# Performance work log

Measured on AMD Instinct MI355X. Metric: run time of the kernel, lower is better.

## Reference

```python
import jax, jax.numpy as jnp
import numpy as np

NUM_CLASSES = 2
THRESHOLD = 0.35
NEGPOS_RATIO = 3
VAR0, VAR1 = 0.1, 0.2
ALPHA = 1.0
B, P, G = 16, 131072, 64


def _iou(a, b):
    # a: [G,4] point-form gts, b: [P,4] point-form priors -> [G,P]
    tl = jnp.maximum(a[:, None, :2], b[None, :, :2])
    br = jnp.minimum(a[:, None, 2:], b[None, :, 2:])
    wh = jnp.clip(br - tl, 0.0)
    inter = wh[..., 0] * wh[..., 1]
    area_a = (a[:, 2] - a[:, 0]) * (a[:, 3] - a[:, 1])
    area_b = (b[:, 2] - b[:, 0]) * (b[:, 3] - b[:, 1])
    return inter / (area_a[:, None] + area_b[None, :] - inter)


def setup_inputs() -> dict:
    key = jax.random.key(0)
    k1, k2, k3, k4, k5, k6 = jax.random.split(key, 6)
    loc_preds = jax.random.normal(k1, (B, P, 4), jnp.float32)
    cls_preds = jax.random.normal(k2, (B, P, NUM_CLASSES), jnp.float32)
    # priors in center form [cx, cy, w, h]
    pcxy = jax.random.uniform(k3, (P, 2), jnp.float32)
    pwh = 0.02 + 0.15 * jax.random.uniform(k4, (P, 2), jnp.float32)
    priorbox = jnp.concatenate([pcxy, pwh], axis=1)
    # ground-truth boxes; stored as [y1,x1,y2,x2,label] so that the module's
    # column permutation [1,0,3,2] yields valid point-form [x1,y1,x2,y2]
    xy1 = 0.8 * jax.random.uniform(k5, (B, G, 2), jnp.float32)
    wh = 0.02 + 0.1 * jax.random.uniform(k6, (B, G, 2), jnp.float32)
    xy2 = xy1 + wh
    boxes_perm = jnp.stack([xy1[..., 1], xy1[..., 0], xy2[..., 1], xy2[..., 0]], axis=-1)
    labels = jnp.ones((B, G, 1), jnp.float32)  # single foreground class (face)
    targets = jnp.concatenate([boxes_perm, labels], axis=-1)
    return {"loc_preds": loc_preds, "cls_preds": cls_preds,
            "priorbox": priorbox, "targets": targets}


def _loss(loc_preds, cls_preds, priorbox, targets):
    priors_c = priorbox[: loc_preds.shape[1], :]
    priors_pt = jnp.concatenate(
        [priors_c[:, :2] - priors_c[:, 2:] / 2,
         priors_c[:, :2] + priors_c[:, 2:] / 2], axis=1)
    num_g = targets.shape[1]

    def match_one(t):
        gts = t[:, :4][:, jnp.array([1, 0, 3, 2])]  # -> point form [x1,y1,x2,y2]
        labels = t[:, 4]
        ov = _iou(gts, priors_pt)                    # [G,P]
        best_prior_idx = jnp.argmax(ov, axis=1)      # [G]
        bto = jnp.max(ov, axis=0)                    # [P] best gt overlap per prior
        bti = jnp.argmax(ov, axis=0)                 # [P]
        bto = bto.at[best_prior_idx].set(2.0)        # force best prior per gt
        bti = bti.at[best_prior_idx].set(jnp.arange(num_g))
        conf = jnp.where(bto < THRESHOLD, 0.0, labels[bti])
        m = gts[bti]                                 # [P,4] matched gt boxes
        g_cxcy = ((m[:, :2] + m[:, 2:]) / 2 - priors_c[:, :2]) / (VAR0 * priors_c[:, 2:])
        g_wh = jnp.log((m[:, 2:] - m[:, :2]) / priors_c[:, 2:]) / VAR1
        return conf, jnp.concatenate([g_cxcy, g_wh], axis=1)

    cls_batch, loc_batch = jax.vmap(match_one)(targets)
    cls_batch = jax.lax.stop_gradient(cls_batch)   # targets require no grad
    loc_batch = jax.lax.stop_gradient(loc_batch)

    pos = cls_batch > 0                              # [B,P]
    npos = jnp.sum(pos)

    # smooth-L1 over positive priors, mean over selected elements (size_average)
    d = loc_preds - loc_batch
    ad = jnp.abs(d)
    sl1 = jnp.where(ad < 1.0, 0.5 * d * d, ad - 0.5)
    loss_loc = jnp.sum(sl1 * pos[..., None]) / jnp.maximum(npos * 4, 1).astype(sl1.dtype)

    # per-prior CE loss for hard-negative mining
    ignore = cls_batch < 0
    lbl = jnp.where(ignore, 0.0, cls_batch).astype(jnp.int32)
    lse = jax.nn.logsumexp(cls_preds, axis=-1)       # [B,P]
    gathered = jnp.take_along_axis(cls_preds, lbl[..., None], axis=-1)[..., 0]
    loss_c = jnp.where(pos | ignore, 0.0, lse - gathered)
    # two-stage sort: rank of each prior by descending loss
    loss_idx = jnp.argsort(-loss_c, axis=1)
    idx_rank = jnp.argsort(loss_idx, axis=1)
    num_pos_img = jnp.sum(pos, axis=1, keepdims=True)
    num_neg = jnp.minimum(NEGPOS_RATIO * num_pos_img, pos.shape[1] - 1)
    neg = idx_rank < num_neg
    mask = pos | neg
    # cross-entropy over mined samples, mean over selected (size_average)
    loss_cls = jnp.sum((lse - gathered) * mask) / jnp.maximum(jnp.sum(mask), 1).astype(lse.dtype)

    loss = (loss_cls + ALPHA * loss_loc) / npos.astype(lse.dtype)
    return loss, loss_loc, loss_cls


def reference(loc_preds, cls_preds, priorbox, targets):
    return _loss(loc_preds, cls_preds, priorbox, targets)
```

## Files before the change

kernel.cpp:

```cpp
#include <hip/hip_runtime.h>

#define BB 16
#define PP 131072
#define GG 64
#define THRESH 0.35f
#define RMAX 0.086f
#define NCH 32
#define CPR 4096
#define NCT 16
#define CPT 8192

#define OFF_BESTP   0
#define OFF_H1TOT   262144
#define OFF_NPOSP   524288
#define OFF_PCP     526336
#define OFF_LOCP    528384
#define OFF_CIDX    530432
#define OFF_NEGS    530496
#define OFF_ARR     530560
#define OFF_DONE    530624
#define OFF_RESN    530688
#define OFF_RESK    530752
#define OFF_RESC    530816
#define OFF_RESL    530880
#define OFF_PU8     530944
#define OFF_KEYS    2628096
#define OFF_CAND    11016704

__global__ __launch_bounds__(1024, 8) void k_match(
    const float* __restrict__ priorbox, const float* __restrict__ targets,
    unsigned long long* __restrict__ bestp, unsigned char* __restrict__ pu8,
    unsigned* __restrict__ h1tot)
{
    __shared__ unsigned msk[8192];
    __shared__ float4 gxy[GG];
    __shared__ unsigned long long sbest[GG];
    const int b = blockIdx.y, chunk = blockIdx.x, tid = threadIdx.x;

    if (tid < 128) h1tot[b * 4096 + chunk * 128 + tid] = 0u;
    for (int i = tid; i < 8192; i += 1024) msk[i] = 0u;
    if (tid < GG) {
        const float* t = targets + (size_t)(b * GG + tid) * 5;
        gxy[tid] = make_float4(t[1], t[0], t[3], t[2]);
        sbest[tid] = 0ull;
    }
    __syncthreads();

    {
        const int g = tid & 63, strip = tid >> 6;
        float4 a = gxy[g];
        int cx0 = max(0, (int)((a.x - RMAX) * 64.f));
        int cx1 = min(63, (int)ceilf((a.z + RMAX) * 64.f) - 1);
        int cy0 = max(0, (int)((a.y - RMAX) * 64.f));
        int cy1 = min(63, (int)ceilf((a.w + RMAX) * 64.f) - 1);
        unsigned bit = 1u << (g & 31);
        const int word = (g >> 5);
        for (int cy = cy0 + strip; cy <= cy1; cy += 16)
            for (int cx = cx0; cx <= cx1; cx++)
                atomicOr(&msk[2 * (cy * 64 + cx) + word], bit);
    }
    __syncthreads();

#pragma unroll
    for (int j = 0; j < 4; j++) {
        const int p = chunk * CPR + j * 1024 + tid;
        float4 pr = *reinterpret_cast<const float4*>(priorbox + (size_t)p * 4);
        float hx = 0.5f * pr.z, hy = 0.5f * pr.w;
        float px1 = pr.x - hx, py1 = pr.y - hy;
        float px2 = pr.x + hx, py2 = pr.y + hy;
        float par = (px2 - px1) * (py2 - py1);
        int cx = min(63, max(0, (int)(pr.x * 64.f)));
        int cy = min(63, max(0, (int)(pr.y * 64.f)));
        uint2 mm = *reinterpret_cast<uint2*>(&msk[2 * (cy * 64 + cx)]);
        unsigned long long m = ((unsigned long long)mm.y << 32) | mm.x;
        const unsigned long long notp = (unsigned long long)(~(unsigned)p);
        float bv = -1.f; int bg = 0;
        while (m) {
            const int g0 = __ffsll(m) - 1; m &= m - 1;
            const bool has1 = (m != 0ull);
            const int g1 = has1 ? (__ffsll(m) - 1) : g0;
            if (has1) m &= m - 1;
            float4 a0 = gxy[g0];
            float4 a1 = gxy[g1];
            float w0 = fmaxf(fminf(a0.z, px2) - fmaxf(a0.x, px1), 0.f);
            float h0 = fmaxf(fminf(a0.w, py2) - fmaxf(a0.y, py1), 0.f);
            float w1 = fmaxf(fminf(a1.z, px2) - fmaxf(a1.x, px1), 0.f);
            float h1 = fmaxf(fminf(a1.w, py2) - fmaxf(a1.y, py1), 0.f);
            float ar0 = (a0.z - a0.x) * (a0.w - a0.y);
            float ar1 = (a1.z - a1.x) * (a1.w - a1.y);
            float i0 = w0 * h0, i1 = w1 * h1;
            float v0 = i0 * __builtin_amdgcn_rcpf(ar0 + par - i0);
            float v1 = i1 * __builtin_amdgcn_rcpf(ar1 + par - i1);
            if (v0 > bv) { bv = v0; bg = g0; }
            if (has1 && v1 > bv) { bv = v1; bg = g1; }
            if (v0 > 0.f)
                atomicMax(&sbest[g0],
                          (((unsigned long long)__float_as_uint(v0)) << 32) | notp);
            if (has1 && v1 > 0.f)
                atomicMax(&sbest[g1],
                          (((unsigned long long)__float_as_uint(v1)) << 32) | notp);
        }
        pu8[(size_t)b * PP + p] = (unsigned char)(bg | ((bv >= THRESH) ? 0x80 : 0));
    }

    __syncthreads();
    if (tid < GG) bestp[(b * NCH + chunk) * GG + tid] = sbest[tid];
}

__global__ __launch_bounds__(1024, 8) void k_loss(
    const float* __restrict__ loc_preds, const float* __restrict__ cls_preds,
    const float* __restrict__ priorbox, const float* __restrict__ targets,
    const unsigned long long* __restrict__ bestp, const unsigned char* __restrict__ pu8,
    unsigned* __restrict__ keys, unsigned* __restrict__ h1tot,
    int* __restrict__ nposp, float* __restrict__ pcp, float* __restrict__ locp,
    unsigned* __restrict__ cidx, float* __restrict__ negs,
    unsigned* __restrict__ arr, unsigned* __restrict__ done)
{
    __shared__ unsigned long long tmp64[2048];
    __shared__ unsigned hcnt[4096];
    __shared__ unsigned char ovr[CPR];
    __shared__ float4 gxy[GG];
    __shared__ float glab[GG];
    __shared__ float sred[32];
    __shared__ int sredi[16];
    const int b = blockIdx.y, chunk = blockIdx.x, tid = threadIdx.x;
    const int lane = tid & 63, wid = tid >> 6;

    if (tid == 0 && chunk == 0) {
        cidx[b] = 0u; negs[b] = 0.f; arr[b] = 0u;
        if (b == 0) *done = 0u;
    }

    tmp64[tid]        = bestp[(b * NCH + (tid >> 6)) * GG + (tid & 63)];
    tmp64[tid + 1024] = bestp[(b * NCH + 16 + (tid >> 6)) * GG + (tid & 63)];
    for (int i = tid; i < 4096; i += 1024) { hcnt[i] = 0u; ovr[i] = 0xFF; }
    if (tid < GG) {
        const float* t = targets + (size_t)(b * GG + tid) * 5;
        gxy[tid] = make_float4(t[1], t[0], t[3], t[2]);
        glab[tid] = t[4];
    }
    __syncthreads();
    for (int s = 16; s > 0; s >>= 1) {
        if (tid < s * 64) {
            const int c = tid >> 6, g = tid & 63;
            unsigned long long a = tmp64[c * 64 + g], d = tmp64[(c + s) * 64 + g];
            tmp64[c * 64 + g] = d > a ? d : a;
        }
        __syncthreads();
    }
    if (tid == 0) {
        for (int g = 0; g < GG; g++) {
            unsigned long long m = tmp64[g];
            if (m) {
                unsigned p = ~((unsigned)(m & 0xFFFFFFFFull));
                if ((int)(p >> 12) == chunk) ovr[p & (CPR - 1)] = (unsigned char)g;
            }
        }
    }
    __syncthreads();

    float locpart = 0.f, clspart = 0.f; int cnt = 0;
#pragma unroll
    for (int j = 0; j < 4; j++) {
        const int plocal = j * 1024 + tid;
        const size_t ip = (size_t)b * PP + chunk * CPR + plocal;
        const unsigned m8 = pu8[ip];
        int g = m8 & 63;
        bool pos = (m8 >> 7) != 0;
        const unsigned o = ovr[plocal];
        if (o != 0xFFu) { pos = true; g = (int)o; }
        const float2 cl = *reinterpret_cast<const float2*>(cls_preds + ip * 2);
        const float mx = fmaxf(cl.x, cl.y);
        const float lse = mx + log1pf(expf(fminf(cl.x, cl.y) - mx));
        unsigned key = 0u;
        if (pos && glab[g] > 0.f) {
            float gathered = (((int)glab[g]) == 0) ? cl.x : cl.y;
            clspart += lse - gathered;
            cnt++;
            const int p = chunk * CPR + plocal;
            float4 pr = *reinterpret_cast<const float4*>(priorbox + (size_t)p * 4);
            float4 gt = gxy[g];
            float gcx = ((gt.x + gt.z) * 0.5f - pr.x) / (0.1f * pr.z);
            float gcy = ((gt.y + gt.w) * 0.5f - pr.y) / (0.1f * pr.w);
            float gw = logf((gt.z - gt.x) / pr.z) / 0.2f;
            float gh = logf((gt.w - gt.y) / pr.w) / 0.2f;
            float4 lp = *reinterpret_cast<const float4*>(loc_preds + ip * 4);
            float d0 = lp.x - gcx, d1 = lp.y - gcy, d2 = lp.z - gw, d3 = lp.w - gh;
            float a0 = fabsf(d0), a1 = fabsf(d1), a2 = fabsf(d2), a3 = fabsf(d3);
            locpart += ((a0 < 1.f) ? 0.5f * d0 * d0 : a0 - 0.5f)
                     + ((a1 < 1.f) ? 0.5f * d1 * d1 : a1 - 0.5f)
                     + ((a2 < 1.f) ? 0.5f * d2 * d2 : a2 - 0.5f)
                     + ((a3 < 1.f) ? 0.5f * d3 * d3 : a3 - 0.5f);
        } else {
            float lc = lse - cl.x;
            key = __float_as_uint(lc);
            atomicAdd(&hcnt[key >> 20], 1u);
        }
        keys[ip] = key;
    }

    for (int o = 32; o; o >>= 1) {
        locpart += __shfl_xor(locpart, o);
        clspart += __shfl_xor(clspart, o);
        cnt     += __shfl_xor(cnt, o);
    }
    if (lane == 0) { sred[wid] = locpart; sred[16 + wid] = clspart; sredi[wid] = cnt; }
    __syncthreads();
    if (tid == 0) {
        float l = 0.f, c = 0.f; int n = 0;
        for (int i = 0; i < 16; i++) { l += sred[i]; c += sred[16 + i]; n += sredi[i]; }
        nposp[b * NCH + chunk] = n;
        pcp[b * NCH + chunk] = c;
        locp[b * NCH + chunk] = l;
    }
    __syncthreads();
    for (int i = tid; i < 4096; i += 1024) {
        unsigned cc = hcnt[i];
        if (cc) atomicAdd(&h1tot[b * 4096 + i], cc);
    }
}

template <int NBINS>
__device__ void find_kth_par(const unsigned* __restrict__ h, int k, int* sel, int* krem)
{
    constexpr int PER = NBINS / 1024;
    __shared__ unsigned wsum_[16];
    __shared__ int res_[2];
    const int tid = threadIdx.x, lane = tid & 63, wid = tid >> 6;
    __syncthreads();
    unsigned own[PER];
    unsigned s = 0;
#pragma unroll
    for (int i = 0; i < PER; i++) { own[i] = h[NBINS - 1 - (tid * PER + i)]; s += own[i]; }
    unsigned incl = s;
    for (int d = 1; d < 64; d <<= 1) {
        unsigned t = __shfl_up(incl, d);
        if (lane >= d) incl += t;
    }
    if (lane == 63) wsum_[wid] = incl;
    if (tid == 0) { res_[0] = -1; res_[1] = 0; }
    __syncthreads();
    unsigned woff = 0;
    for (int w = 0; w < 16; w++) woff += (w < wid) ? wsum_[w] : 0u;
    const unsigned texcl = woff + incl - s;
    if (k > 0 && texcl < (unsigned)k && texcl + s >= (unsigned)k) {
        unsigned run = texcl;
#pragma unroll
        for (int i = 0; i < PER; i++) {
            run += own[i];
            if (run >= (unsigned)k) {
                res_[0] = NBINS - 1 - (tid * PER + i);
                res_[1] = k - (int)(run - own[i]);
                break;
            }
        }
    }
    __syncthreads();
    *sel = res_[0]; *krem = res_[1];
}

__device__ float block_sum_f(float v)
{
    __shared__ float rs[16];
    const int tid = threadIdx.x;
    __syncthreads();
    for (int o = 32; o; o >>= 1) v += __shfl_xor(v, o);
    if ((tid & 63) == 0) rs[tid >> 6] = v;
    __syncthreads();
    float s = 0.f;
    for (int i = 0; i < 16; i++) s += rs[i];
    return s;
}

__global__ __launch_bounds__(1024) void k_tail(
    const unsigned* __restrict__ keys, const unsigned* __restrict__ h1tot,
    const int* __restrict__ nposp, const float* __restrict__ pcp,
    const float* __restrict__ locp, unsigned* __restrict__ cand,
    unsigned* __restrict__ cidx, float* __restrict__ negs,
    unsigned* __restrict__ arr, unsigned* __restrict__ done,
    int* __restrict__ resn, int* __restrict__ resk,
    float* __restrict__ resc, float* __restrict__ resl, float* __restrict__ out)
{
    __shared__ unsigned wcnt[16], wbase[16];
    __shared__ unsigned bbase;
    __shared__ int snp, lastflag;
    __shared__ unsigned ch[1024];
    __shared__ float cs[1024];
    const int b = blockIdx.y, chunk = blockIdx.x, tid = threadIdx.x;
    const int lane = tid & 63, wid = tid >> 6;

    if (tid == 0) {
        int np = 0;
        for (int c = 0; c < NCH; c++) np += nposp[b * NCH + c];
        snp = np;
    }
    unsigned kv[8];
#pragma unroll
    for (int j = 0; j < 8; j++)
        kv[j] = keys[(size_t)b * PP + chunk * CPT + j * 1024 + tid];
    __syncthreads();
    const int np = snp;
    const int k = min(3 * np, PP - 1);
    int sel1, kk1;
    find_kth_par<4096>(h1tot + b * 4096, k, &sel1, &kk1);
    const unsigned s1 = (unsigned)sel1;

    float nv = 0.f;
    if (sel1 >= 0) {
#pragma unroll
        for (int j = 0; j < 8; j++)
            if ((kv[j] >> 20) > s1) nv += __uint_as_float(kv[j]);
    }
    float nsum = block_sum_f(nv);
    if (tid == 0 && nsum != 0.f) atomicAdd(&negs[b], nsum);

    unsigned long long mv[8];
    unsigned wn = 0;
#pragma unroll
    for (int j = 0; j < 8; j++) {
        mv[j] = __ballot((kv[j] >> 20) == s1);
        wn += (unsigned)__popcll(mv[j]);
    }
    if (lane == 0) wcnt[wid] = wn;
    __syncthreads();
    if (tid == 0) {
        unsigned run = 0;
        for (int w = 0; w < 16; w++) { wbase[w] = run; run += wcnt[w]; }
        bbase = run ? atomicAdd(&cidx[b], run) : 0u;
    }
    __syncthreads();
    {
        unsigned run = bbase + wbase[wid];
        const unsigned long long lanemask = (1ull << lane) - 1ull;
#pragma unroll
        for (int j = 0; j < 8; j++) {
            if ((kv[j] >> 20) == s1)
                cand[(size_t)b * PP + run + (unsigned)__popcll(mv[j] & lanemask)] = kv[j];
            run += (unsigned)__popcll(mv[j]);
        }
    }

    __syncthreads();
    if (tid == 0) {
        __threadfence();
        unsigned old = atomicAdd(&arr[b], 1u);
        lastflag = (old == NCT - 1) ? 1 : 0;
    }
    __syncthreads();
    if (!lastflag) return;
    if (tid == 0) __threadfence();
    __syncthreads();

    const unsigned ncand = cidx[b];
    ch[tid] = 0u; cs[tid] = 0.f;
    __syncthreads();
    for (unsigned i = tid; i < ncand; i += 1024) {
        unsigned v = cand[(size_t)b * PP + i];
        unsigned bin = (v >> 10) & 1023u;
        atomicAdd(&ch[bin], 1u);
        atomicAdd(&cs[bin], __uint_as_float(v));
    }
    __syncthreads();
    int sel2, kk2;
    find_kth_par<1024>(ch, (sel1 < 0) ? 0 : kk1, &sel2, &kk2);
    float sumhi2 = block_sum_f((sel2 >= 0 && tid > sel2) ? cs[tid] : 0.f);

    __syncthreads();
    ch[tid] = 0u; cs[tid] = 0.f;
    __syncthreads();
    if (sel2 >= 0) {
        for (unsigned i = tid; i < ncand; i += 1024) {
            unsigned v = cand[(size_t)b * PP + i];
            if (((v >> 10) & 1023u) == (unsigned)sel2) {
                atomicAdd(&ch[v & 1023u], 1u);
                atomicAdd(&cs[v & 1023u], __uint_as_float(v));
            }
        }
    }
    __syncthreads();
    int sel3, needeq;
    find_kth_par<1024>(ch, (sel2 < 0) ? 0 : kk2, &sel3, &needeq);
    float sumhi3 = block_sum_f((sel3 >= 0 && tid > sel3) ? cs[tid] : 0.f);

    if (tid == 0) {
        float pcsum = 0.f, locsum = 0.f;
        for (int c = 0; c < NCH; c++) {
            pcsum += pcp[b * NCH + c];
            locsum += locp[b * NCH + c];
        }
        float add = 0.f;
        if (sel3 >= 0 && needeq > 0) {
            unsigned Kstar = ((unsigned)sel1 << 20) | ((unsigned)sel2 << 10) | (unsigned)sel3;
            add = needeq * __uint_as_float(Kstar);
        }
        resn[b] = np;
        resk[b] = k;
        resc[b] = pcsum + negs[b] + sumhi2 + sumhi3 + add;
        resl[b] = locsum;
        __threadfence();
        unsigned old = atomicAdd(done, 1u);
        lastflag = (old == BB - 1) ? 1 : 0;
    }
    __syncthreads();
    if (!lastflag || tid != 0) return;

    __threadfence();
    volatile int* vrn = (volatile int*)resn;
    volatile int* vrk = (volatile int*)resk;
    volatile float* vrc = (volatile float*)resc;
    volatile float* vrl = (volatile float*)resl;
    int npt = 0; long long maskc = 0; float clsnum = 0.f, locnum = 0.f;
    for (int b2 = 0; b2 < BB; b2++) {
        npt += vrn[b2];
        maskc += (long long)vrn[b2] + vrk[b2];
        clsnum += vrc[b2];
        locnum += vrl[b2];
    }
    float denom_loc = (float)((4 * npt > 1) ? 4 * npt : 1);
    float denom_cls = (float)((maskc > 1) ? maskc : 1);
    float loss_loc = locnum / denom_loc;
    float loss_cls = clsnum / denom_cls;
    out[0] = (loss_cls + loss_loc) / (float)npt;
    out[1] = loss_loc;
    out[2] = loss_cls;
}

extern "C" void kernel_launch(void* const* d_in, const int* in_sizes, int n_in,
                              void* d_out, int out_size, void* d_ws, size_t ws_size,
                              hipStream_t stream)
{
    const float* loc_preds = (const float*)d_in[0];
    const float* cls_preds = (const float*)d_in[1];
    const float* priorbox  = (const float*)d_in[2];
    const float* targets   = (const float*)d_in[3];
    float* out = (float*)d_out;

    char* ws = (char*)d_ws;
    unsigned long long* bestp = (unsigned long long*)(ws + OFF_BESTP);
    unsigned* h1tot = (unsigned*)(ws + OFF_H1TOT);
    int*      nposp = (int*)(ws + OFF_NPOSP);
    float*    pcp   = (float*)(ws + OFF_PCP);
    float*    locp  = (float*)(ws + OFF_LOCP);
    unsigned* cidx  = (unsigned*)(ws + OFF_CIDX);
    float*    negs  = (float*)(ws + OFF_NEGS);
    unsigned* arr   = (unsigned*)(ws + OFF_ARR);
    unsigned* done  = (unsigned*)(ws + OFF_DONE);
    int*      resn  = (int*)(ws + OFF_RESN);
    int*      resk  = (int*)(ws + OFF_RESK);
    float*    resc  = (float*)(ws + OFF_RESC);
    float*    resl  = (float*)(ws + OFF_RESL);
    unsigned char* pu8 = (unsigned char*)(ws + OFF_PU8);
    unsigned* keys  = (unsigned*)(ws + OFF_KEYS);
    unsigned* cand  = (unsigned*)(ws + OFF_CAND);

    k_match<<<dim3(NCH, BB), 1024, 0, stream>>>(priorbox, targets, bestp, pu8, h1tot);
    k_loss<<<dim3(NCH, BB), 1024, 0, stream>>>(loc_preds, cls_preds, priorbox, targets,
                                               bestp, pu8, keys, h1tot,
                                               nposp, pcp, locp, cidx, negs, arr, done);
    k_tail<<<dim3(NCT, BB), 1024, 0, stream>>>(keys, h1tot, nposp, pcp, locp, cand,
                                               cidx, negs, arr, done,
                                               resn, resk, resc, resl, out);
}
```

Measured before the change: 96.74 us.

## Split tail into separate kernels, shrink blocks to 256, coarsen match grid

Reworks the pipeline from three 1024-thread kernels into six smaller launches. k_match and k_loss move to 256-thread blocks over 64 chunks, and the match grid cell count drops from 64 to 32. The per-chunk best-prior reduction moves into a dedicated k_bred kernel. The last-block-done atomics in the tail are replaced by separate compact, select and final kernels. The aim is to improve occupancy and remove serial per-block reductions and atomic handshakes, at the cost of extra launch overhead and more IoU candidates per coarser grid cell.

```diff
diff --git a/kernel.cpp b/kernel.cpp
--- a/kernel.cpp
+++ b/kernel.cpp
@@ -5,40 +5,44 @@
 #define GG 64
 #define THRESH 0.35f
 #define RMAX 0.086f
-#define NCH 32
-#define CPR 4096
-#define NCT 16
-#define CPT 8192
+#define NCELL 32
+#define NCHM 64
+#define CPM 2048
+#define NCHL 64
+#define CPL 2048
+#define NCC 64
+#define CPC 2048
 
 #define OFF_BESTP   0
-#define OFF_H1TOT   262144
-#define OFF_NPOSP   524288
-#define OFF_PCP     526336
-#define OFF_LOCP    528384
-#define OFF_CIDX    530432
-#define OFF_NEGS    530496
-#define OFF_ARR     530560
-#define OFF_DONE    530624
-#define OFF_RESN    530688
-#define OFF_RESK    530752
-#define OFF_RESC    530816
-#define OFF_RESL    530880
-#define OFF_PU8     530944
-#define OFF_KEYS    2628096
-#define OFF_CAND    11016704
-
-__global__ __launch_bounds__(1024, 8) void k_match(
+#define OFF_BEST64  524288
+#define OFF_H1TOT   532480
+#define OFF_NPOSP   794624
+#define OFF_PCP     798720
+#define OFF_LOCP    802816
+#define OFF_CIDX    806912
+#define OFF_NEGS    806976
+#define OFF_RESN    807040
+#define OFF_RESK    807104
+#define OFF_RESC    807168
+#define OFF_RESL    807232
+#define OFF_PU8     807296
+#define OFF_KEYS    2904448
+#define OFF_CAND    11293056
+
+__global__ __launch_bounds__(256) void k_match(
     const float* __restrict__ priorbox, const float* __restrict__ targets,
     unsigned long long* __restrict__ bestp, unsigned char* __restrict__ pu8,
-    unsigned* __restrict__ h1tot)
-{
-    __shared__ unsigned msk[8192];
+    unsigned* __restrict__ h1tot, unsigned* __restrict__ cidx,
+    float* __restrict__ negs)
+{
+    __shared__ unsigned msk[2 * NCELL * NCELL];
     __shared__ float4 gxy[GG];
     __shared__ unsigned long long sbest[GG];
     const int b = blockIdx.y, chunk = blockIdx.x, tid = threadIdx.x;
 
-    if (tid < 128) h1tot[b * 4096 + chunk * 128 + tid] = 0u;
-    for (int i = tid; i < 8192; i += 1024) msk[i] = 0u;
+    if (tid < 64) h1tot[b * 4096 + chunk * 64 + tid] = 0u;
+    if (chunk == 0 && tid == 0) { cidx[b] = 0u; negs[b] = 0.f; }
+    for (int i = tid; i < 2 * NCELL * NCELL; i += 256) msk[i] = 0u;
     if (tid < GG) {
         const float* t = targets + (size_t)(b * GG + tid) * 5;
         gxy[tid] = make_float4(t[1], t[0], t[3], t[2]);
@@ -49,29 +53,29 @@
     {
         const int g = tid & 63, strip = tid >> 6;
         float4 a = gxy[g];
-        int cx0 = max(0, (int)((a.x - RMAX) * 64.f));
-        int cx1 = min(63, (int)ceilf((a.z + RMAX) * 64.f) - 1);
-        int cy0 = max(0, (int)((a.y - RMAX) * 64.f));
-        int cy1 = min(63, (int)ceilf((a.w + RMAX) * 64.f) - 1);
+        int cx0 = max(0, (int)((a.x - RMAX) * (float)NCELL));
+        int cx1 = min(NCELL - 1, (int)ceilf((a.z + RMAX) * (float)NCELL) - 1);
+        int cy0 = max(0, (int)((a.y - RMAX) * (float)NCELL));
+        int cy1 = min(NCELL - 1, (int)ceilf((a.w + RMAX) * (float)NCELL) - 1);
         unsigned bit = 1u << (g & 31);
         const int word = (g >> 5);
-        for (int cy = cy0 + strip; cy <= cy1; cy += 16)
+        for (int cy = cy0 + strip; cy <= cy1; cy += 4)
             for (int cx = cx0; cx <= cx1; cx++)
-                atomicOr(&msk[2 * (cy * 64 + cx) + word], bit);
-    }
-    __syncthreads();
-
-#pragma unroll
-    for (int j = 0; j < 4; j++) {
-        const int p = chunk * CPR + j * 1024 + tid;
+                atomicOr(&msk[2 * (cy * NCELL + cx) + word], bit);
+    }
+    __syncthreads();
+
+#pragma unroll
+    for (int j = 0; j < 8; j++) {
+        const int p = chunk * CPM + j * 256 + tid;
         float4 pr = *reinterpret_cast<const float4*>(priorbox + (size_t)p * 4);
         float hx = 0.5f * pr.z, hy = 0.5f * pr.w;
         float px1 = pr.x - hx, py1 = pr.y - hy;
         float px2 = pr.x + hx, py2 = pr.y + hy;
         float par = (px2 - px1) * (py2 - py1);
-        int cx = min(63, max(0, (int)(pr.x * 64.f)));
-        int cy = min(63, max(0, (int)(pr.y * 64.f)));
-        uint2 mm = *reinterpret_cast<uint2*>(&msk[2 * (cy * 64 + cx)]);
+        int cx = min(NCELL - 1, max(0, (int)(pr.x * (float)NCELL)));
+        int cy = min(NCELL - 1, max(0, (int)(pr.y * (float)NCELL)));
+        uint2 mm = *reinterpret_cast<uint2*>(&msk[2 * (cy * NCELL + cx)]);
         unsigned long long m = ((unsigned long long)mm.y << 32) | mm.x;
         const unsigned long long notp = (unsigned long long)(~(unsigned)p);
         float bv = -1.f; int bg = 0;
@@ -104,71 +108,66 @@
     }
 
     __syncthreads();
-    if (tid < GG) bestp[(b * NCH + chunk) * GG + tid] = sbest[tid];
-}
-
-__global__ __launch_bounds__(1024, 8) void k_loss(
+    if (tid < GG) bestp[(b * NCHM + chunk) * GG + tid] = sbest[tid];
+}
+
+__global__ void k_bred(const unsigned long long* __restrict__ bestp,
+                       unsigned long long* __restrict__ best64)
+{
+    const int b = blockIdx.x, g = threadIdx.x;
+    unsigned long long m = 0ull;
+#pragma unroll 8
+    for (int c = 0; c < NCHM; c++) {
+        unsigned long long v = bestp[(b * NCHM + c) * GG + g];
+        m = v > m ? v : m;
+    }
+    best64[b * GG + g] = m;
+}
+
+__global__ __launch_bounds__(256) void k_loss(
     const float* __restrict__ loc_preds, const float* __restrict__ cls_preds,
     const float* __restrict__ priorbox, const float* __restrict__ targets,
-    const unsigned long long* __restrict__ bestp, const unsigned char* __restrict__ pu8,
+    const unsigned long long* __restrict__ best64, const unsigned char* __restrict__ pu8,
     unsigned* __restrict__ keys, unsigned* __restrict__ h1tot,
-    int* __restrict__ nposp, float* __restrict__ pcp, float* __restrict__ locp,
-    unsigned* __restrict__ cidx, float* __restrict__ negs,
-    unsigned* __restrict__ arr, unsigned* __restrict__ done)
-{
-    __shared__ unsigned long long tmp64[2048];
+    int* __restrict__ nposp, float* __restrict__ pcp, float* __restrict__ locp)
+{
     __shared__ unsigned hcnt[4096];
-    __shared__ unsigned char ovr[CPR];
+    __shared__ unsigned ovr[CPL];
     __shared__ float4 gxy[GG];
     __shared__ float glab[GG];
-    __shared__ float sred[32];
-    __shared__ int sredi[16];
+    __shared__ float sred[8];
+    __shared__ int sredi[4];
     const int b = blockIdx.y, chunk = blockIdx.x, tid = threadIdx.x;
     const int lane = tid & 63, wid = tid >> 6;
 
-    if (tid == 0 && chunk == 0) {
-        cidx[b] = 0u; negs[b] = 0.f; arr[b] = 0u;
-        if (b == 0) *done = 0u;
-    }
-
-    tmp64[tid]        = bestp[(b * NCH + (tid >> 6)) * GG + (tid & 63)];
-    tmp64[tid + 1024] = bestp[(b * NCH + 16 + (tid >> 6)) * GG + (tid & 63)];
-    for (int i = tid; i < 4096; i += 1024) { hcnt[i] = 0u; ovr[i] = 0xFF; }
+    for (int i = tid; i < 4096; i += 256) hcnt[i] = 0u;
+    for (int i = tid; i < CPL; i += 256) ovr[i] = 0u;
     if (tid < GG) {
         const float* t = targets + (size_t)(b * GG + tid) * 5;
         gxy[tid] = make_float4(t[1], t[0], t[3], t[2]);
         glab[tid] = t[4];
     }
     __syncthreads();
-    for (int s = 16; s > 0; s >>= 1) {
-        if (tid < s * 64) {
-            const int c = tid >> 6, g = tid & 63;
-            unsigned long long a = tmp64[c * 64 + g], d = tmp64[(c + s) * 64 + g];
-            tmp64[c * 64 + g] = d > a ? d : a;
-        }
-        __syncthreads();
-    }
-    if (tid == 0) {
-        for (int g = 0; g < GG; g++) {
-            unsigned long long m = tmp64[g];
-            if (m) {
-                unsigned p = ~((unsigned)(m & 0xFFFFFFFFull));
-                if ((int)(p >> 12) == chunk) ovr[p & (CPR - 1)] = (unsigned char)g;
-            }
+    if (tid < GG) {
+        unsigned long long m = best64[b * GG + tid];
+        if (m) {
+            unsigned p = ~((unsigned)(m & 0xFFFFFFFFull));
+            if ((int)(p >> 11) == chunk)
+                atomicMax(&ovr[p & (CPL - 1)], (unsigned)tid + 1u);
         }
     }
     __syncthreads();
 
     float locpart = 0.f, clspart = 0.f; int cnt = 0;
 #pragma unroll
-    for (int j = 0; j < 4; j++) {
-        const int plocal = j * 1024 + tid;
-        const size_t ip = (size_t)b * PP + chunk * CPR + plocal;
+    for (int j = 0; j < 8; j++) {
+        const int plocal = j * 256 + tid;
+        const size_t ip = (size_t)b * PP + chunk * CPL + plocal;
         const unsigned m8 = pu8[ip];
         int g = m8 & 63;
         bool pos = (m8 >> 7) != 0;
         const unsigned o = ovr[plocal];
-        if (o != 0xFFu) { pos = true; g = (int)o; }
+        if (o) { pos = true; g = (int)o - 1; }
         const float2 cl = *reinterpret_cast<const float2*>(cls_preds + ip * 2);
         const float mx = fmaxf(cl.x, cl.y);
         const float lse = mx + log1pf(expf(fminf(cl.x, cl.y) - mx));
@@ -177,7 +176,7 @@
             float gathered = (((int)glab[g]) == 0) ? cl.x : cl.y;
             clspart += lse - gathered;
             cnt++;
-            const int p = chunk * CPR + plocal;
+            const int p = chunk * CPL + plocal;
             float4 pr = *reinterpret_cast<const float4*>(priorbox + (size_t)p * 4);
             float4 gt = gxy[g];
             float gcx = ((gt.x + gt.z) * 0.5f - pr.x) / (0.1f * pr.z);
@@ -204,17 +203,18 @@
         clspart += __shfl_xor(clspart, o);
         cnt     += __shfl_xor(cnt, o);
     }
-    if (lane == 0) { sred[wid] = locpart; sred[16 + wid] = clspart; sredi[wid] = cnt; }
+    if (lane == 0) { sred[wid] = locpart; sred[4 + wid] = clspart; sredi[wid] = cnt; }
     __syncthreads();
     if (tid == 0) {
-        float l = 0.f, c = 0.f; int n = 0;
-        for (int i = 0; i < 16; i++) { l += sred[i]; c += sred[16 + i]; n += sredi[i]; }
-        nposp[b * NCH + chunk] = n;
-        pcp[b * NCH + chunk] = c;
-        locp[b * NCH + chunk] = l;
-    }
-    __syncthreads();
-    for (int i = tid; i < 4096; i += 1024) {
+        float l = sred[0] + sred[1] + sred[2] + sred[3];
+        float c = sred[4] + sred[5] + sred[6] + sred[7];
+        int n = sredi[0] + sredi[1] + sredi[2] + sredi[3];
+        nposp[b * NCHL + chunk] = n;
+        pcp[b * NCHL + chunk] = c;
+        locp[b * NCHL + chunk] = l;
+    }
+    __syncthreads();
+    for (int i = tid; i < 4096; i += 256) {
         unsigned cc = hcnt[i];
         if (cc) atomicAdd(&h1tot[b * 4096 + i], cc);
     }
@@ -223,15 +223,14 @@
 template <int NBINS>
 __device__ void find_kth_par(const unsigned* __restrict__ h, int k, int* sel, int* krem)
 {
-    constexpr int PER = NBINS / 1024;
-    __shared__ unsigned wsum_[16];
+    constexpr int PER = NBINS / 256;
+    __shared__ unsigned wsum_[4];
     __shared__ int res_[2];
     const int tid = threadIdx.x, lane = tid & 63, wid = tid >> 6;
     __syncthreads();
-    unsigned own[PER];
     unsigned s = 0;
 #pragma unroll
-    for (int i = 0; i < PER; i++) { own[i] = h[NBINS - 1 - (tid * PER + i)]; s += own[i]; }
+    for (int i = 0; i < PER; i++) s += h[NBINS - 1 - (tid * PER + i)];
     unsigned incl = s;
     for (int d = 1; d < 64; d <<= 1) {
         unsigned t = __shfl_up(incl, d);
@@ -241,16 +240,16 @@
     if (tid == 0) { res_[0] = -1; res_[1] = 0; }
     __syncthreads();
     unsigned woff = 0;
-    for (int w = 0; w < 16; w++) woff += (w < wid) ? wsum_[w] : 0u;
+    for (int w = 0; w < 4; w++) woff += (w < wid) ? wsum_[w] : 0u;
     const unsigned texcl = woff + incl - s;
     if (k > 0 && texcl < (unsigned)k && texcl + s >= (unsigned)k) {
         unsigned run = texcl;
-#pragma unroll
         for (int i = 0; i < PER; i++) {
-            run += own[i];
+            unsigned hv = h[NBINS - 1 - (tid * PER + i)];
+            run += hv;
             if (run >= (unsigned)k) {
                 res_[0] = NBINS - 1 - (tid * PER + i);
-                res_[1] = k - (int)(run - own[i]);
+                res_[1] = k - (int)(run - hv);
                 break;
             }
         }
@@ -261,45 +260,44 @@
 
 __device__ float block_sum_f(float v)
 {
-    __shared__ float rs[16];
+    __shared__ float rs[4];
     const int tid = threadIdx.x;
     __syncthreads();
     for (int o = 32; o; o >>= 1) v += __shfl_xor(v, o);
     if ((tid & 63) == 0) rs[tid >> 6] = v;
     __syncthreads();
-    float s = 0.f;
-    for (int i = 0; i < 16; i++) s += rs[i];
-    return s;
-}
-
-__global__ __launch_bounds__(1024) void k_tail(
+    return rs[0] + rs[1] + rs[2] + rs[3];
+}
+
+__device__ int np_of_image(const int* __restrict__ nposp, int b)
+{
+    __shared__ int snp;
+    const int tid = threadIdx.x;
+    int v = (tid < 64) ? nposp[b * NCHL + tid] : 0;
+    if (tid < 64) {
+        for (int o = 32; o; o >>= 1) v += __shfl_xor(v, o);
+        if (tid == 0) snp = v;
+    }
+    __syncthreads();
+    return snp;
+}
+
+__global__ __launch_bounds__(256) void k_compact(
     const unsigned* __restrict__ keys, const unsigned* __restrict__ h1tot,
-    const int* __restrict__ nposp, const float* __restrict__ pcp,
-    const float* __restrict__ locp, unsigned* __restrict__ cand,
-    unsigned* __restrict__ cidx, float* __restrict__ negs,
-    unsigned* __restrict__ arr, unsigned* __restrict__ done,
-    int* __restrict__ resn, int* __restrict__ resk,
-    float* __restrict__ resc, float* __restrict__ resl, float* __restrict__ out)
-{
-    __shared__ unsigned wcnt[16], wbase[16];
+    const int* __restrict__ nposp, unsigned* __restrict__ cand,
+    unsigned* __restrict__ cidx, float* __restrict__ negs)
+{
+    __shared__ unsigned wcnt[4], wbase[4];
     __shared__ unsigned bbase;
-    __shared__ int snp, lastflag;
-    __shared__ unsigned ch[1024];
-    __shared__ float cs[1024];
     const int b = blockIdx.y, chunk = blockIdx.x, tid = threadIdx.x;
     const int lane = tid & 63, wid = tid >> 6;
 
-    if (tid == 0) {
-        int np = 0;
-        for (int c = 0; c < NCH; c++) np += nposp[b * NCH + c];
-        snp = np;
-    }
     unsigned kv[8];
 #pragma unroll
     for (int j = 0; j < 8; j++)
-        kv[j] = keys[(size_t)b * PP + chunk * CPT + j * 1024 + tid];
-    __syncthreads();
-    const int np = snp;
+        kv[j] = keys[(size_t)b * PP + chunk * CPC + j * 256 + tid];
+
+    const int np = np_of_image(nposp, b);
     const int k = min(3 * np, PP - 1);
     int sel1, kk1;
     find_kth_par<4096>(h1tot + b * 4096, k, &sel1, &kk1);
@@ -325,36 +323,46 @@
     __syncthreads();
     if (tid == 0) {
         unsigned run = 0;
-        for (int w = 0; w < 16; w++) { wbase[w] = run; run += wcnt[w]; }
+        for (int w = 0; w < 4; w++) { wbase[w] = run; run += wcnt[w]; }
         bbase = run ? atomicAdd(&cidx[b], run) : 0u;
     }
     __syncthreads();
-    {
-        unsigned run = bbase + wbase[wid];
-        const unsigned long long lanemask = (1ull << lane) - 1ull;
-#pragma unroll
-        for (int j = 0; j < 8; j++) {
-            if ((kv[j] >> 20) == s1)
-                cand[(size_t)b * PP + run + (unsigned)__popcll(mv[j] & lanemask)] = kv[j];
-            run += (unsigned)__popcll(mv[j]);
-        }
-    }
-
-    __syncthreads();
-    if (tid == 0) {
-        __threadfence();
-        unsigned old = atomicAdd(&arr[b], 1u);
-        lastflag = (old == NCT - 1) ? 1 : 0;
-    }
-    __syncthreads();
-    if (!lastflag) return;
-    if (tid == 0) __threadfence();
-    __syncthreads();
-
+    unsigned run = bbase + wbase[wid];
+    const unsigned long long lanemask = (1ull << lane) - 1ull;
+#pragma unroll
+    for (int j = 0; j < 8; j++) {
+        if ((kv[j] >> 20) == s1)
+            cand[(size_t)b * PP + run + (unsigned)__popcll(mv[j] & lanemask)] = kv[j];
+        run += (unsigned)__popcll(mv[j]);
+    }
+}
+
+__global__ __launch_bounds__(256) void k_select(
+    const unsigned* __restrict__ cand, const unsigned* __restrict__ cidx,
+    const unsigned* __restrict__ h1tot, const int* __restrict__ nposp,
+    const float* __restrict__ pcp, const float* __restrict__ locp,
+    const float* __restrict__ negs,
+    int* __restrict__ resn, int* __restrict__ resk,
+    float* __restrict__ resc, float* __restrict__ resl)
+{
+    __shared__ unsigned ch[1024];
+    __shared__ float cs[1024];
+    const int b = blockIdx.x, tid = threadIdx.x;
+
+    const int np = np_of_image(nposp, b);
+    const int k = min(3 * np, PP - 1);
+    int sel1, kk1;
+    find_kth_par<4096>(h1tot + b * 4096, k, &sel1, &kk1);
     const unsigned ncand = cidx[b];
-    ch[tid] = 0u; cs[tid] = 0.f;
-    __syncthreads();
-    for (unsigned i = tid; i < ncand; i += 1024) {
+
+    float pv = (tid < 64) ? pcp[b * NCHL + tid] : 0.f;
+    float lv = (tid < 64) ? locp[b * NCHL + tid] : 0.f;
+    float pcsum = block_sum_f(pv);
+    float locsum = block_sum_f(lv);
+
+    for (int i = tid; i < 1024; i += 256) { ch[i] = 0u; cs[i] = 0.f; }
+    __syncthreads();
+    for (unsigned i = tid; i < ncand; i += 256) {
         unsigned v = cand[(size_t)b * PP + i];
         unsigned bin = (v >> 10) & 1023u;
         atomicAdd(&ch[bin], 1u);
@@ -363,13 +371,16 @@
     __syncthreads();
     int sel2, kk2;
     find_kth_par<1024>(ch, (sel1 < 0) ? 0 : kk1, &sel2, &kk2);
-    float sumhi2 = block_sum_f((sel2 >= 0 && tid > sel2) ? cs[tid] : 0.f);
-
-    __syncthreads();
-    ch[tid] = 0u; cs[tid] = 0.f;
+    float s2v = 0.f;
+    for (int i = tid * 4; i < tid * 4 + 4; i++)
+        if (sel2 >= 0 && i > sel2) s2v += cs[i];
+    float sumhi2 = block_sum_f(s2v);
+
+    __syncthreads();
+    for (int i = tid; i < 1024; i += 256) { ch[i] = 0u; cs[i] = 0.f; }
     __syncthreads();
     if (sel2 >= 0) {
-        for (unsigned i = tid; i < ncand; i += 1024) {
+        for (unsigned i = tid; i < ncand; i += 256) {
             unsigned v = cand[(size_t)b * PP + i];
             if (((v >> 10) & 1023u) == (unsigned)sel2) {
                 atomicAdd(&ch[v & 1023u], 1u);
@@ -380,14 +391,12 @@
     __syncthreads();
     int sel3, needeq;
     find_kth_par<1024>(ch, (sel2 < 0) ? 0 : kk2, &sel3, &needeq);
-    float sumhi3 = block_sum_f((sel3 >= 0 && tid > sel3) ? cs[tid] : 0.f);
+    float s3v = 0.f;
+    for (int i = tid * 4; i < tid * 4 + 4; i++)
+        if (sel3 >= 0 && i > sel3) s3v += cs[i];
+    float sumhi3 = block_sum_f(s3v);
 
     if (tid == 0) {
-        float pcsum = 0.f, locsum = 0.f;
-        for (int c = 0; c < NCH; c++) {
-            pcsum += pcp[b * NCH + c];
-            locsum += locp[b * NCH + c];
-        }
         float add = 0.f;
         if (sel3 >= 0 && needeq > 0) {
             unsigned Kstar = ((unsigned)sel1 << 20) | ((unsigned)sel2 << 10) | (unsigned)sel3;
@@ -397,32 +406,30 @@
         resk[b] = k;
         resc[b] = pcsum + negs[b] + sumhi2 + sumhi3 + add;
         resl[b] = locsum;
-        __threadfence();
-        unsigned old = atomicAdd(done, 1u);
-        lastflag = (old == BB - 1) ? 1 : 0;
-    }
-    __syncthreads();
-    if (!lastflag || tid != 0) return;
-
-    __threadfence();
-    volatile int* vrn = (volatile int*)resn;
-    volatile int* vrk = (volatile int*)resk;
-    volatile float* vrc = (volatile float*)resc;
-    volatile float* vrl = (volatile float*)resl;
-    int npt = 0; long long maskc = 0; float clsnum = 0.f, locnum = 0.f;
-    for (int b2 = 0; b2 < BB; b2++) {
-        npt += vrn[b2];
-        maskc += (long long)vrn[b2] + vrk[b2];
-        clsnum += vrc[b2];
-        locnum += vrl[b2];
-    }
-    float denom_loc = (float)((4 * npt > 1) ? 4 * npt : 1);
-    float denom_cls = (float)((maskc > 1) ? maskc : 1);
-    float loss_loc = locnum / denom_loc;
-    float loss_cls = clsnum / denom_cls;
-    out[0] = (loss_cls + loss_loc) / (float)npt;
-    out[1] = loss_loc;
-    out[2] = loss_cls;
+    }
+}
+
+__global__ void k_final(const int* __restrict__ resn, const int* __restrict__ resk,
+                        const float* __restrict__ resc, const float* __restrict__ resl,
+                        float* __restrict__ out)
+{
+    const int t = threadIdx.x;
+    int n = 0, kk = 0; float c = 0.f, l = 0.f;
+    if (t < BB) { n = resn[t]; kk = resk[t]; c = resc[t]; l = resl[t]; }
+    for (int o = 8; o; o >>= 1) {
+        n += __shfl_xor(n, o); kk += __shfl_xor(kk, o);
+        c += __shfl_xor(c, o); l += __shfl_xor(l, o);
+    }
+    if (t == 0) {
+        long long maskc = (long long)n + kk;
+        float denom_loc = (float)((4 * n > 1) ? 4 * n : 1);
+        float denom_cls = (float)((maskc > 1) ? maskc : 1);
+        float loss_loc = l / denom_loc;
+        float loss_cls = c / denom_cls;
+        out[0] = (loss_cls + loss_loc) / (float)n;
+        out[1] = loss_loc;
+        out[2] = loss_cls;
+    }
 }
 
 extern "C" void kernel_launch(void* const* d_in, const int* in_sizes, int n_in,
@@ -436,15 +443,14 @@
     float* out = (float*)d_out;
 
     char* ws = (char*)d_ws;
-    unsigned long long* bestp = (unsigned long long*)(ws + OFF_BESTP);
+    unsigned long long* bestp  = (unsigned long long*)(ws + OFF_BESTP);
+    unsigned long long* best64 = (unsigned long long*)(ws + OFF_BEST64);
     unsigned* h1tot = (unsigned*)(ws + OFF_H1TOT);
     int*      nposp = (int*)(ws + OFF_NPOSP);
     float*    pcp   = (float*)(ws + OFF_PCP);
     float*    locp  = (float*)(ws + OFF_LOCP);
     unsigned* cidx  = (unsigned*)(ws + OFF_CIDX);
     float*    negs  = (float*)(ws + OFF_NEGS);
-    unsigned* arr   = (unsigned*)(ws + OFF_ARR);
-    unsigned* done  = (unsigned*)(ws + OFF_DONE);
     int*      resn  = (int*)(ws + OFF_RESN);
     int*      resk  = (int*)(ws + OFF_RESK);
     float*    resc  = (float*)(ws + OFF_RESC);
@@ -453,11 +459,14 @@
     unsigned* keys  = (unsigned*)(ws + OFF_KEYS);
     unsigned* cand  = (unsigned*)(ws + OFF_CAND);
 
-    k_match<<<dim3(NCH, BB), 1024, 0, stream>>>(priorbox, targets, bestp, pu8, h1tot);
-    k_loss<<<dim3(NCH, BB), 1024, 0, stream>>>(loc_preds, cls_preds, priorbox, targets,
-                                               bestp, pu8, keys, h1tot,
-                                               nposp, pcp, locp, cidx, negs, arr, done);
-    k_tail<<<dim3(NCT, BB), 1024, 0, stream>>>(keys, h1tot, nposp, pcp, locp, cand,
-                                               cidx, negs, arr, done,
-                                               resn, resk, resc, resl, out);
-}
+    k_match<<<dim3(NCHM, BB), 256, 0, stream>>>(priorbox, targets, bestp, pu8,
+                                                h1tot, cidx, negs);
+    k_bred<<<BB, 64, 0, stream>>>(bestp, best64);
+    k_loss<<<dim3(NCHL, BB), 256, 0, stream>>>(loc_preds, cls_preds, priorbox, targets,
+                                               best64, pu8, keys, h1tot,
+                                               nposp, pcp, locp);
+    k_compact<<<dim3(NCC, BB), 256, 0, stream>>>(keys, h1tot, nposp, cand, cidx, negs);
+    k_select<<<BB, 256, 0, stream>>>(cand, cidx, h1tot, nposp, pcp, locp, negs,
+                                     resn, resk, resc, resl);
+    k_final<<<1, 64, 0, stream>>>(resn, resk, resc, resl, out);
+}
```

After: 100.5 us. 1.04x slower.
